# Kernel optimization log

Hardware: AMD Instinct MI355X
Metric: run time of the kernel (lower is better)

## Reference

```python
import jax, jax.numpy as jnp
import numpy as np

H = W = 128  # render resolution (init height/width)
EPS = 1e-8

def _normalize(x, axis):
    return x / (jnp.linalg.norm(x, axis=axis, keepdims=True) + EPS)

def _render_one(pts, camrot, campos, proj, uv, faces):
    # pts (p,3), camrot (3,3), campos (3,), proj (3,1), uv (p,2), faces (f,3)
    pc = (pts - campos) @ camrot.T                       # camera-space verts (p,3)
    xy = pc[:, :2] * proj[:2, 0] / (pc[:, 2:3] + EPS)    # perspective projection -> NDC (p,2)
    v3d = pc[faces]                                      # (f,3,3)
    v2d = xy[faces]                                      # (f,3,2)
    n = jnp.cross(v3d[:, 1] - v3d[:, 0], v3d[:, 2] - v3d[:, 0])  # face normals (f,3)
    n1 = _normalize(n, axis=1)
    # pixel grid in NDC
    px = jnp.linspace(-1.0, 1.0, W)[None, None, :]
    py = jnp.linspace(1.0, -1.0, H)[None, :, None]
    ax, ay = v2d[:, 0, 0, None, None], v2d[:, 0, 1, None, None]
    bx, by = v2d[:, 1, 0, None, None], v2d[:, 1, 1, None, None]
    cx, cy = v2d[:, 2, 0, None, None], v2d[:, 2, 1, None, None]
    d = (by - cy) * (ax - cx) + (cx - bx) * (ay - cy)    # (f,1,1) signed 2*area
    l0 = ((by - cy) * (px - cx) + (cx - bx) * (py - cy)) / (d + EPS)
    l1 = ((cy - ay) * (px - cx) + (ax - cx) * (py - cy)) / (d + EPS)
    l2 = 1.0 - l0 - l1                                   # barycentrics (f,H,W)
    z = (l0 * v3d[:, 0, 2, None, None] + l1 * v3d[:, 1, 2, None, None]
         + l2 * v3d[:, 2, 2, None, None])                # interpolated depth (f,H,W)
    inside = (l0 >= 0) & (l1 >= 0) & (l2 >= 0) & (jnp.abs(d) > EPS) & (z > EPS)
    zm = jnp.where(inside, z, jnp.float32(1e10))
    idx = jnp.argmin(zm, axis=0)                         # nearest visible face per pixel (H,W)
    hard = jnp.any(inside, axis=0)[..., None].astype(pts.dtype)  # hardmask (H,W,1)
    take = lambda a: jnp.take_along_axis(a, idx[None], axis=0)[0]  # (H,W)
    uvsel = uv[faces][idx]                               # (H,W,3,2) per-pixel face uvs
    tc = (take(l0)[..., None] * uvsel[..., 0, :]
          + take(l1)[..., None] * uvsel[..., 1, :]
          + take(l2)[..., None] * uvsel[..., 2, :]) * hard  # imtexcoords (H,W,2)
    return tc, hard, n1

def _fragment_shader(tc, texture, mask):
    # nearest-filter texture lookup; texture (3,th,tw)
    th, tw = texture.shape[1], texture.shape[2]
    u = jnp.clip(tc[..., 0], 0.0, 1.0)
    v = jnp.clip(tc[..., 1], 0.0, 1.0)
    tx = jnp.round(u * (tw - 1)).astype(jnp.int32)
    ty = jnp.round((1.0 - v) * (th - 1)).astype(jnp.int32)
    color = texture[:, ty, tx].transpose(1, 2, 0)        # (H,W,3)
    return color * mask

def setup_inputs() -> dict:
    key = jax.random.key(0)
    ks = jax.random.split(key, 6)
    b, p, f = 3, 768, 1024
    points = jax.random.normal(ks[0], (b, p, 3), jnp.float32) * 0.3
    faces = jax.random.randint(ks[1], (f, 3), 0, p)
    camera_rot = jnp.broadcast_to(jnp.eye(3, dtype=jnp.float32), (b, 3, 3))
    camera_pos = jnp.zeros((b, 3), jnp.float32).at[:, 2].set(-3.0)  # objects in front of camera
    camera_proj = jnp.ones((3, 1), jnp.float32)
    uv = jax.random.uniform(ks[2], (b, p, 2), jnp.float32)
    texture = jax.random.uniform(ks[3], (b, 3, 512, 512), jnp.float32)
    ts = jax.random.normal(ks[4], (b, 3), jnp.float32)
    return dict(points=points, camera_rot=camera_rot, camera_pos=camera_pos,
                camera_proj=camera_proj, uv=uv, texture=texture, ts=ts, faces=faces)

def reference(points, camera_rot, camera_pos, camera_proj, uv, texture, ts, faces):
    b = points.shape[0]
    render = jax.vmap(_render_one, in_axes=(0, 0, 0, None, 0, None))
    tcs, masks, normals = render(points, camera_rot, camera_pos, camera_proj, uv, faces)
    ims = jax.vmap(_fragment_shader)(tcs, texture, masks)   # (b,H,W,3)
    probs = masks                                            # improb proxy == hardmask
    order = jnp.argsort(-ts[:, 2])                           # far -> near compositing order
    ims_s, probs_s, masks_s = ims[order], probs[order], masks[order]
    imrender, improb, fg = ims_s[0], probs_s[0], masks_s[0]
    for i in range(1, b):                                    # fixed small layer count
        m = masks_s[i] > 0.5
        imrender = jnp.where(m, ims_s[i], imrender)
        improb = jnp.where(m, probs_s[i], improb)
        fg = jnp.where(m, masks_s[i], fg)
    return imrender[None], improb[None], normals, fg[None]
```

## Files before the change

kernel.cpp:

```cpp
#include <hip/hip_runtime.h>
#include <math.h>

#define B_ 3
#define P_ 768
#define F_ 1024
#define H_ 128
#define W_ 128
#define HW_ (H_*W_)
#define EPS_ 1e-8f

#define OFF_PROB   49152
#define OFF_NORM   65536
#define OFF_FG     74752


__global__ __launch_bounds__(256) void raster_fwd(
    const float* __restrict__ points,
    const float* __restrict__ camrot,
    const float* __restrict__ campos,
    const float* __restrict__ proj,
    const int*   __restrict__ faces,
    float4* __restrict__ faceA,
    float4* __restrict__ faceB,
    unsigned long long* __restrict__ packed,
    float*  __restrict__ normals_out)
{
#pragma clang fp contract(off)
    int wid  = blockIdx.x * 4 + (threadIdx.x >> 6);
    int lane = threadIdx.x & 63;
    int b = wid / F_;
    int f = wid - b * F_;

    const float* R = camrot + b * 9;
    float cpx = campos[b*3+0], cpy = campos[b*3+1], cpz = campos[b*3+2];
    float pj0 = proj[0], pj1 = proj[1];

    float pcx[3], pcy[3], pcz[3], sx[3], sy[3];
    for (int v = 0; v < 3; ++v) {
        int vi = faces[f*3 + v];
        const float* P = points + (b*P_ + vi) * 3;
        float vx = P[0] - cpx;
        float vy = P[1] - cpy;
        float vz = P[2] - cpz;
        float qx = (vx*R[0] + vy*R[1]) + vz*R[2];
        float qy = (vx*R[3] + vy*R[4]) + vz*R[5];
        float qz = (vx*R[6] + vy*R[7]) + vz*R[8];
        pcx[v] = qx; pcy[v] = qy; pcz[v] = qz;
        float dz = qz + EPS_;
        sx[v] = (qx * pj0) / dz;
        sy[v] = (qy * pj1) / dz;
    }

    float ax = sx[0], ay = sy[0];
    float bx = sx[1], by = sy[1];
    float cx = sx[2], cy = sy[2];

    float e0x = by - cy;
    float e0y = cx - bx;
    float e1x = cy - ay;
    float e1y = ax - cx;
    float d = e0x*(ax - cx) + e0y*(ay - cy);
    float denom = d + EPS_;
    bool valid = fabsf(d) > EPS_;
    float z0 = pcz[0], z1 = pcz[1], z2 = pcz[2];

    if (lane == 0) {
        faceA[wid] = make_float4(e0x, e0y, e1x, e1y);
        faceB[wid] = make_float4(cx, cy, denom, valid ? 1.0f : 0.0f);

        float ux = pcx[1]-pcx[0], uy = pcy[1]-pcy[0], uz = pcz[1]-pcz[0];
        float wx = pcx[2]-pcx[0], wy = pcy[2]-pcy[0], wz = pcz[2]-pcz[0];
        float nx = fmaf(uy, wz, -(uz*wy));
        float ny = fmaf(uz, wx, -(ux*wz));
        float nz = fmaf(ux, wy, -(uy*wx));
        float nn = sqrtf((nx*nx + ny*ny) + nz*nz) + 1e-8f;
        normals_out[wid*3+0] = nx / nn;
        normals_out[wid*3+1] = ny / nn;
        normals_out[wid*3+2] = nz / nn;
    }

    if (!valid) return;

    float gx0 = (ax + 1.0f) * 63.5f;
    float gx1 = (bx + 1.0f) * 63.5f;
    float gx2 = (cx + 1.0f) * 63.5f;
    float gy0 = (1.0f - ay) * 63.5f;
    float gy1 = (1.0f - by) * 63.5f;
    float gy2 = (1.0f - cy) * 63.5f;
    int xlo = max(0,   (int)ceilf (fminf(fminf(gx0,gx1),gx2) - 1.0f));
    int xhi = min(127, (int)floorf(fmaxf(fmaxf(gx0,gx1),gx2) + 1.0f));
    int ylo = max(0,   (int)ceilf (fminf(fminf(gy0,gy1),gy2) - 1.0f));
    int yhi = min(127, (int)floorf(fmaxf(fmaxf(gy0,gy1),gy2) + 1.0f));
    int wX = xhi - xlo + 1;
    int wY = yhi - ylo + 1;
    if (wX <= 0 || wY <= 0) return;
    int N = wX * wY;

    int q64 = 64 / wX;
    int r64 = 64 - q64 * wX;
    int yy = lane / wX;
    int xx = lane - yy * wX;

    const double STEP = 2.0 / 127.0;
    unsigned long long* cells = packed + b * HW_;

    for (int i = lane; i < N; i += 64) {
        int X = xlo + xx;
        int Y = ylo + yy;
        float px = (float)(-1.0 + (double)X * STEP);
        float py = (float)( 1.0 - (double)Y * STEP);
        float dx = px - cx;
        float dy = py - cy;
        float n0 = e0x*dx + e0y*dy;
        float n1 = e1x*dx + e1y*dy;
        float l0 = n0 / denom;
        float l1 = n1 / denom;
        float l2 = 1.0f - l0 - l1;
        float zz = (l0*z0 + l1*z1) + l2*z2;
        if (l0 >= 0.0f && l1 >= 0.0f && l2 >= 0.0f && zz > EPS_) {
            unsigned long long pk =
                ((unsigned long long)__float_as_uint(zz) << 32) | (unsigned)f;
            atomicMin(&cells[Y * W_ + X], pk);
        }
        xx += r64; yy += q64;
        if (xx >= wX) { xx -= wX; yy += 1; }
    }
}

__global__ __launch_bounds__(128) void shade_composite(
    const float4* __restrict__ faceA,
    const float4* __restrict__ faceB,
    const int*    __restrict__ faces,
    const float*  __restrict__ uv,
    const float*  __restrict__ tex,
    const float*  __restrict__ ts,
    const unsigned long long* __restrict__ packed,
    float* __restrict__ out)
{
#pragma clang fp contract(off)
    int pix = blockIdx.x * 128 + threadIdx.x;
    int y = pix >> 7;
    int x = pix & (W_ - 1);

    const double STEP = 2.0 / 127.0;
    float px = (float)(-1.0 + (double)x * STEP);
    float py = (float)( 1.0 - (double)y * STEP);

    const unsigned MISS_BITS = __float_as_uint(1e10f);

    unsigned long long pk0 = packed[0 * HW_ + pix];
    unsigned long long pk1 = packed[1 * HW_ + pix];
    unsigned long long pk2 = packed[2 * HW_ + pix];
    unsigned long long pks[B_] = {pk0, pk1, pk2};

    float rr[B_], gg[B_], bb_[B_], mm[B_];
    for (int b = 0; b < B_; ++b) {
        unsigned long long pk = pks[b];
        unsigned zbits = (unsigned)(pk >> 32);
        bool hard = zbits < MISS_BITS;
        float r = 0.0f, g = 0.0f, bl = 0.0f, m = 0.0f;
        if (hard) {
            m = 1.0f;
            int fi = (int)(unsigned)pk;
            float4 A = faceA[b * F_ + fi];
            float4 Bv = faceB[b * F_ + fi];
            float dx = px - Bv.x;
            float dy = py - Bv.y;
            float n0 = A.x*dx + A.y*dy;
            float n1 = A.z*dx + A.w*dy;
            float l0 = n0 / Bv.z;
            float l1 = n1 / Bv.z;
            float l2 = 1.0f - l0 - l1;

            int i0 = faces[fi*3+0];
            int i1 = faces[fi*3+1];
            int i2 = faces[fi*3+2];
            const float* uvb = uv + b * P_ * 2;
            float u0 = uvb[i0*2+0], v0 = uvb[i0*2+1];
            float u1 = uvb[i1*2+0], v1 = uvb[i1*2+1];
            float u2 = uvb[i2*2+0], v2 = uvb[i2*2+1];
            float tu = (l0*u0 + l1*u1) + l2*u2;
            float tv = (l0*v0 + l1*v1) + l2*v2;
            float uc = fminf(fmaxf(tu, 0.0f), 1.0f);
            float vc = fminf(fmaxf(tv, 0.0f), 1.0f);
            int txi = (int)rintf(uc * 511.0f);
            int tyi = (int)rintf((1.0f - vc) * 511.0f);
            const float* tb = tex + b * 3 * 512 * 512;
            r  = tb[(0*512 + tyi)*512 + txi];
            g  = tb[(1*512 + tyi)*512 + txi];
            bl = tb[(2*512 + tyi)*512 + txi];
        }
        rr[b] = r; gg[b] = g; bb_[b] = bl; mm[b] = m;
    }

    float k0 = ts[0*3+2], k1 = ts[1*3+2], k2 = ts[2*3+2];
    int o0 = 0, o1 = 1, o2 = 2;
    if (k1 > k0) { int ti=o0; o0=o1; o1=ti; float tf=k0; k0=k1; k1=tf; }
    if (k2 > k1) { int ti=o1; o1=o2; o2=ti; float tf=k1; k1=k2; k2=tf; }
    if (k1 > k0) { int ti=o0; o0=o1; o1=ti; float tf=k0; k0=k1; k1=tf; }

    float sr = rr[o0], sg = gg[o0], sb = bb_[o0], sm = mm[o0];
    if (mm[o1] > 0.5f) { sr = rr[o1]; sg = gg[o1]; sb = bb_[o1]; sm = mm[o1]; }
    if (mm[o2] > 0.5f) { sr = rr[o2]; sg = gg[o2]; sb = bb_[o2]; sm = mm[o2]; }

    out[pix*3+0] = sr;
    out[pix*3+1] = sg;
    out[pix*3+2] = sb;
    out[OFF_PROB + pix] = sm;
    out[OFF_FG   + pix] = sm;
}

extern "C" void kernel_launch(void* const* d_in, const int* in_sizes, int n_in,
                              void* d_out, int out_size, void* d_ws, size_t ws_size,
                              hipStream_t stream) {
    const float* points = (const float*)d_in[0];
    const float* camrot = (const float*)d_in[1];
    const float* campos = (const float*)d_in[2];
    const float* proj   = (const float*)d_in[3];
    const float* uv     = (const float*)d_in[4];
    const float* tex    = (const float*)d_in[5];
    const float* ts     = (const float*)d_in[6];
    const int*   faces  = (const int*)d_in[7];
    float* out = (float*)d_out;

    char* ws = (char*)d_ws;
    float4* faceA = (float4*)(ws);
    float4* faceB = (float4*)(ws + 49152);
    unsigned long long* packed = (unsigned long long*)(ws + 98304);

    hipMemsetAsync(packed, 0xFF, (size_t)B_ * HW_ * 8, stream);

    raster_fwd<<<dim3(B_*F_/4), dim3(256), 0, stream>>>(
        points, camrot, campos, proj, faces, faceA, faceB, packed,
        out + OFF_NORM);
    shade_composite<<<dim3(HW_/128), dim3(128), 0, stream>>>(
        faceA, faceB, faces, uv, tex, ts, packed, out);
}
```

Before: 88.82 us.

## Precompute per-face UVs, split raster pixels across two wave groups, branchless shading loads

The raster kernel now writes each face's three vertex UVs into new workspace arrays (faceC/faceD). The shading kernel therefore reads them directly instead of chasing faces->uv indirections. Raster launches a second grid dimension so two waves share a face's bounding-box pixels, which halves per-wave serial iterations at the cost of duplicated setup work. The shade kernel issues all per-layer face loads unconditionally (face index 0 on miss) and masks the texture samples, so more loads are in flight at the expense of extra memory traffic for missed pixels.

```diff
diff --git a/kernel.cpp b/kernel.cpp
--- a/kernel.cpp
+++ b/kernel.cpp
@@ -22,11 +22,15 @@
     const int*   __restrict__ faces,
     float4* __restrict__ faceA,
     float4* __restrict__ faceB,
+    float4* __restrict__ faceC,
+    float2* __restrict__ faceD,
+    const float* __restrict__ uv,
     unsigned long long* __restrict__ packed,
     float*  __restrict__ normals_out)
 {
 #pragma clang fp contract(off)
     int wid  = blockIdx.x * 4 + (threadIdx.x >> 6);
+    int sub  = blockIdx.y;
     int lane = threadIdx.x & 63;
     int b = wid / F_;
     int f = wid - b * F_;
@@ -35,9 +39,11 @@
     float cpx = campos[b*3+0], cpy = campos[b*3+1], cpz = campos[b*3+2];
     float pj0 = proj[0], pj1 = proj[1];
 
+    int idx3[3];
     float pcx[3], pcy[3], pcz[3], sx[3], sy[3];
     for (int v = 0; v < 3; ++v) {
         int vi = faces[f*3 + v];
+        idx3[v] = vi;
         const float* P = points + (b*P_ + vi) * 3;
         float vx = P[0] - cpx;
         float vy = P[1] - cpy;
@@ -64,9 +70,13 @@
     bool valid = fabsf(d) > EPS_;
     float z0 = pcz[0], z1 = pcz[1], z2 = pcz[2];
 
-    if (lane == 0) {
+    if (lane == 0 && sub == 0) {
         faceA[wid] = make_float4(e0x, e0y, e1x, e1y);
         faceB[wid] = make_float4(cx, cy, denom, valid ? 1.0f : 0.0f);
+        const float* uvb = uv + b * P_ * 2;
+        faceC[wid] = make_float4(uvb[idx3[0]*2+0], uvb[idx3[0]*2+1],
+                                 uvb[idx3[1]*2+0], uvb[idx3[1]*2+1]);
+        faceD[wid] = make_float2(uvb[idx3[2]*2+0], uvb[idx3[2]*2+1]);
 
         float ux = pcx[1]-pcx[0], uy = pcy[1]-pcy[0], uz = pcz[1]-pcz[0];
         float wx = pcx[2]-pcx[0], wy = pcy[2]-pcy[0], wz = pcz[2]-pcz[0];
@@ -96,15 +106,17 @@
     if (wX <= 0 || wY <= 0) return;
     int N = wX * wY;
 
-    int q64 = 64 / wX;
-    int r64 = 64 - q64 * wX;
-    int yy = lane / wX;
-    int xx = lane - yy * wX;
+    int i0 = sub * 64 + lane;
+    if (i0 >= N) return;
+    int q = 128 / wX;
+    int r = 128 - q * wX;
+    int yy = i0 / wX;
+    int xx = i0 - yy * wX;
 
     const double STEP = 2.0 / 127.0;
     unsigned long long* cells = packed + b * HW_;
 
-    for (int i = lane; i < N; i += 64) {
+    for (int i = i0; i < N; i += 128) {
         int X = xlo + xx;
         int Y = ylo + yy;
         float px = (float)(-1.0 + (double)X * STEP);
@@ -122,7 +134,7 @@
                 ((unsigned long long)__float_as_uint(zz) << 32) | (unsigned)f;
             atomicMin(&cells[Y * W_ + X], pk);
         }
-        xx += r64; yy += q64;
+        xx += r; yy += q;
         if (xx >= wX) { xx -= wX; yy += 1; }
     }
 }
@@ -130,8 +142,8 @@
 __global__ __launch_bounds__(128) void shade_composite(
     const float4* __restrict__ faceA,
     const float4* __restrict__ faceB,
-    const int*    __restrict__ faces,
-    const float*  __restrict__ uv,
+    const float4* __restrict__ faceC,
+    const float2* __restrict__ faceD,
     const float*  __restrict__ tex,
     const float*  __restrict__ ts,
     const unsigned long long* __restrict__ packed,
@@ -148,49 +160,45 @@
 
     const unsigned MISS_BITS = __float_as_uint(1e10f);
 
-    unsigned long long pk0 = packed[0 * HW_ + pix];
-    unsigned long long pk1 = packed[1 * HW_ + pix];
-    unsigned long long pk2 = packed[2 * HW_ + pix];
-    unsigned long long pks[B_] = {pk0, pk1, pk2};
-
-    float rr[B_], gg[B_], bb_[B_], mm[B_];
+    unsigned long long pks[B_];
+    for (int b = 0; b < B_; ++b) pks[b] = packed[b * HW_ + pix];
+
+    float m[B_]; int fi[B_];
+    float4 A[B_], Bv[B_], Cv[B_]; float2 Dv[B_];
     for (int b = 0; b < B_; ++b) {
-        unsigned long long pk = pks[b];
-        unsigned zbits = (unsigned)(pk >> 32);
-        bool hard = zbits < MISS_BITS;
-        float r = 0.0f, g = 0.0f, bl = 0.0f, m = 0.0f;
-        if (hard) {
-            m = 1.0f;
-            int fi = (int)(unsigned)pk;
-            float4 A = faceA[b * F_ + fi];
-            float4 Bv = faceB[b * F_ + fi];
-            float dx = px - Bv.x;
-            float dy = py - Bv.y;
-            float n0 = A.x*dx + A.y*dy;
-            float n1 = A.z*dx + A.w*dy;
-            float l0 = n0 / Bv.z;
-            float l1 = n1 / Bv.z;
-            float l2 = 1.0f - l0 - l1;
-
-            int i0 = faces[fi*3+0];
-            int i1 = faces[fi*3+1];
-            int i2 = faces[fi*3+2];
-            const float* uvb = uv + b * P_ * 2;
-            float u0 = uvb[i0*2+0], v0 = uvb[i0*2+1];
-            float u1 = uvb[i1*2+0], v1 = uvb[i1*2+1];
-            float u2 = uvb[i2*2+0], v2 = uvb[i2*2+1];
-            float tu = (l0*u0 + l1*u1) + l2*u2;
-            float tv = (l0*v0 + l1*v1) + l2*v2;
-            float uc = fminf(fmaxf(tu, 0.0f), 1.0f);
-            float vc = fminf(fmaxf(tv, 0.0f), 1.0f);
-            int txi = (int)rintf(uc * 511.0f);
-            int tyi = (int)rintf((1.0f - vc) * 511.0f);
-            const float* tb = tex + b * 3 * 512 * 512;
-            r  = tb[(0*512 + tyi)*512 + txi];
-            g  = tb[(1*512 + tyi)*512 + txi];
-            bl = tb[(2*512 + tyi)*512 + txi];
-        }
-        rr[b] = r; gg[b] = g; bb_[b] = bl; mm[b] = m;
+        bool hard = (unsigned)(pks[b] >> 32) < MISS_BITS;
+        m[b]  = hard ? 1.0f : 0.0f;
+        fi[b] = hard ? (int)(unsigned)pks[b] : 0;
+        A[b]  = faceA[b * F_ + fi[b]];
+        Bv[b] = faceB[b * F_ + fi[b]];
+        Cv[b] = faceC[b * F_ + fi[b]];
+        Dv[b] = faceD[b * F_ + fi[b]];
+    }
+
+    int txi[B_], tyi[B_];
+    for (int b = 0; b < B_; ++b) {
+        float dx = px - Bv[b].x;
+        float dy = py - Bv[b].y;
+        float n0 = A[b].x*dx + A[b].y*dy;
+        float n1 = A[b].z*dx + A[b].w*dy;
+        float l0 = n0 / Bv[b].z;
+        float l1 = n1 / Bv[b].z;
+        float l2 = 1.0f - l0 - l1;
+        float tu = (l0*Cv[b].x + l1*Cv[b].z) + l2*Dv[b].x;
+        float tv = (l0*Cv[b].y + l1*Cv[b].w) + l2*Dv[b].y;
+        float uc = fminf(fmaxf(tu, 0.0f), 1.0f);
+        float vc = fminf(fmaxf(tv, 0.0f), 1.0f);
+        txi[b] = (int)rintf(uc * 511.0f);
+        tyi[b] = (int)rintf((1.0f - vc) * 511.0f);
+    }
+
+    float rr[B_], gg[B_], bb_[B_];
+    for (int b = 0; b < B_; ++b) {
+        const float* tb = tex + b * 3 * 512 * 512;
+        int o = tyi[b]*512 + txi[b];
+        rr[b]  = tb[0*262144 + o] * m[b];
+        gg[b]  = tb[1*262144 + o] * m[b];
+        bb_[b] = tb[2*262144 + o] * m[b];
     }
 
     float k0 = ts[0*3+2], k1 = ts[1*3+2], k2 = ts[2*3+2];
@@ -199,9 +207,9 @@
     if (k2 > k1) { int ti=o1; o1=o2; o2=ti; float tf=k1; k1=k2; k2=tf; }
     if (k1 > k0) { int ti=o0; o0=o1; o1=ti; float tf=k0; k0=k1; k1=tf; }
 
-    float sr = rr[o0], sg = gg[o0], sb = bb_[o0], sm = mm[o0];
-    if (mm[o1] > 0.5f) { sr = rr[o1]; sg = gg[o1]; sb = bb_[o1]; sm = mm[o1]; }
-    if (mm[o2] > 0.5f) { sr = rr[o2]; sg = gg[o2]; sb = bb_[o2]; sm = mm[o2]; }
+    float sr = rr[o0], sg = gg[o0], sb = bb_[o0], sm = m[o0];
+    if (m[o1] > 0.5f) { sr = rr[o1]; sg = gg[o1]; sb = bb_[o1]; sm = m[o1]; }
+    if (m[o2] > 0.5f) { sr = rr[o2]; sg = gg[o2]; sb = bb_[o2]; sm = m[o2]; }
 
     out[pix*3+0] = sr;
     out[pix*3+1] = sg;
@@ -226,13 +234,15 @@
     char* ws = (char*)d_ws;
     float4* faceA = (float4*)(ws);
     float4* faceB = (float4*)(ws + 49152);
-    unsigned long long* packed = (unsigned long long*)(ws + 98304);
+    float4* faceC = (float4*)(ws + 98304);
+    float2* faceD = (float2*)(ws + 147456);
+    unsigned long long* packed = (unsigned long long*)(ws + 172032);
 
     hipMemsetAsync(packed, 0xFF, (size_t)B_ * HW_ * 8, stream);
 
-    raster_fwd<<<dim3(B_*F_/4), dim3(256), 0, stream>>>(
-        points, camrot, campos, proj, faces, faceA, faceB, packed,
-        out + OFF_NORM);
+    raster_fwd<<<dim3(B_*F_/4, 2), dim3(256), 0, stream>>>(
+        points, camrot, campos, proj, faces, faceA, faceB, faceC, faceD, uv,
+        packed, out + OFF_NORM);
     shade_composite<<<dim3(HW_/128), dim3(128), 0, stream>>>(
-        faceA, faceB, faces, uv, tex, ts, packed, out);
+        faceA, faceB, faceC, faceD, tex, ts, packed, out);
 }
```

Result: no change. 88.51 us (-0.4%).
